# Kernel optimization log

Measured on AMD Instinct MI355X. Metric: run time of the kernel, lower is better.

The kernel has to match this reference:

```python
import jax, jax.numpy as jnp
import numpy as np

HEADS = 16

def setup_inputs() -> dict:
    key = jax.random.key(0)
    k1, k2, k3 = jax.random.split(key, 3)
    b, t, d = 2, 2048, 1024
    x = jax.random.normal(k1, (b, t, d), dtype=jnp.float32)
    w_qkv = jax.random.normal(k2, (d, 3 * d), dtype=jnp.float32) * (d ** -0.5)
    w_out = jax.random.normal(k3, (d, d), dtype=jnp.float32) * (d ** -0.5)
    b_out = jnp.zeros((d,), dtype=jnp.float32)
    return {"x": x, "w_qkv": w_qkv, "w_out": w_out, "b_out": b_out}

def reference(x, w_qkv, w_out, b_out):
    b, t, d = x.shape
    h = HEADS
    dh = d // h
    qkv = x @ w_qkv                      # [b, t, 3d]
    q, k, v = jnp.split(qkv, 3, axis=-1)
    split_heads = lambda a: a.reshape(b, t, h, dh).transpose(0, 2, 1, 3)  # [b,h,t,dh]
    q, k, v = map(split_heads, (q, k, v))
    # NOTE: faithful to source — no 1/sqrt(dh) scaling, causal=False so no mask
    dots = jnp.einsum('bhid,bhjd->bhij', q, k)      # [b,h,t,t]
    attn = jax.nn.softmax(dots, axis=-1)
    out = jnp.einsum('bhjd,bhij->bhid', v, attn)    # [b,h,t,dh]
    out = out.transpose(0, 2, 1, 3).reshape(b, t, d)
    return out @ w_out + b_out
```

## Files before the change

### kernel.cpp

```cpp
#include <hip/hip_runtime.h>
#include <hip/hip_bf16.h>
#include <stdint.h>

typedef __attribute__((ext_vector_type(4))) float f32x4;
typedef __attribute__((ext_vector_type(8))) short bf16x8;

#define MFMA(a, b, c) __builtin_amdgcn_mfma_f32_16x16x32_bf16((a), (b), (c), 0, 0, 0)
#define BAR do { __builtin_amdgcn_s_barrier(); asm volatile("" ::: "memory"); } while (0)

template <int N> __device__ __forceinline__ void waitcnt_vm() {
  if constexpr (N == 0) asm volatile("s_waitcnt vmcnt(0)" ::: "memory");
  else if constexpr (N == 3) asm volatile("s_waitcnt vmcnt(3)" ::: "memory");
  else if constexpr (N == 4) asm volatile("s_waitcnt vmcnt(4)" ::: "memory");
}

__device__ __forceinline__ uint16_t f2b(float f) {
  uint32_t u = __builtin_bit_cast(uint32_t, f);
  uint32_t r = (u + 0x7FFFu + ((u >> 16) & 1u)) >> 16;
  return (uint16_t)r;
}

__device__ __forceinline__ uint32_t cvt_pk_bf16(float lo, float hi) {
  uint32_t r;
  asm("v_cvt_pk_bf16_f32 %0, %1, %2" : "=v"(r) : "v"(lo), "v"(hi));
  return r;
}

__device__ __forceinline__ float fexp2(float x) {
  float r;
  asm("v_exp_f32 %0, %1" : "=v"(r) : "v"(x));
  return r;
}

__device__ __forceinline__ void gld_lds16(const void* g, void* l) {
  __builtin_amdgcn_global_load_lds((const __attribute__((address_space(1))) uint32_t*)g,
                                   (__attribute__((address_space(3))) uint32_t*)l, 16, 0, 0);
}

__device__ __forceinline__ int swz(int r) {
  return (r & 3) | ((((r >> 2) ^ (r >> 3)) & 1) << 2);
}

__global__ __launch_bounds__(256) void cast_bf16(const float* __restrict__ in,
                                                 uint16_t* __restrict__ out, int n) {
  const int i = (blockIdx.x * 256 + threadIdx.x) * 4;
  if (i >= n) return;
  const float4 v = *(const float4*)(in + i);
  ushort4 o;
  o.x = f2b(v.x); o.y = f2b(v.y); o.z = f2b(v.z); o.w = f2b(v.w);
  *(ushort4*)(out + i) = o;
}

__global__ __launch_bounds__(256) void transpose_cast(const float* __restrict__ in,
                                                      uint16_t* __restrict__ out, int R, int C) {
  __shared__ float t_[32][33];
  const int c0 = blockIdx.x * 32, r0 = blockIdx.y * 32;
  const int tx = threadIdx.x & 31, ty = threadIdx.x >> 5;
#pragma unroll
  for (int i = 0; i < 4; i++)
    t_[ty + i * 8][tx] = in[(size_t)(r0 + ty + i * 8) * C + c0 + tx];
  __syncthreads();
#pragma unroll
  for (int i = 0; i < 4; i++)
    out[(size_t)(c0 + ty + i * 8) * R + r0 + tx] = f2b(t_[tx][ty + i * 8]);
}

template <int NOUT, int BN, bool BF16_OUT, bool BIAS, bool SCALEQ, bool VSPLIT>
__global__ __launch_bounds__(256) void gemm_bt(const uint16_t* __restrict__ A,
                                               const uint16_t* __restrict__ Bt,
                                               const float* __restrict__ bias,
                                               void* __restrict__ Cout,
                                               uint16_t* __restrict__ VTout) {
  constexpr int NF = BN / 32;
  constexpr int TILEB = 8192 + BN * 64;
  constexpr int NL = 2 + BN / 64;
  __shared__ __align__(16) char LDS[3 * TILEB];
  const int tid = threadIdx.x;
  const int wave = tid >> 6, lane = tid & 63;
  const int lr = lane & 15, lg = lane >> 4;
  const int row0 = blockIdx.y * 128, col0 = blockIdx.x * BN;
  const int wr = (wave >> 1) * 64, wc = (wave & 1) * (BN / 2);

  f32x4 acc[4][NF] = {};

  const int ldsOff = wave * 1024 + lane * 16;
  const int srow = ldsOff >> 6, scolB = ldsOff & 63;
  const char* ApA = (const char*)A + ((size_t)(row0 + srow) * 1024) * 2 + scolB;
  const char* ApB = ApA + 64 * 2048;
  const char* BpA = (const char*)Bt + ((size_t)(col0 + srow) * 1024) * 2 + scolB;
  const char* BpB = BpA + 64 * 2048;

  auto stage = [&](int t, char* base) {
    char* d = base + wave * 1024;
    const int kk = t * 64;
    gld_lds16(ApA + kk, d);
    gld_lds16(ApB + kk, d + 4096);
    gld_lds16(BpA + kk, d + 8192);
    if constexpr (BN == 128) gld_lds16(BpB + kk, d + 12288);
  };
  auto compute = [&](const char* S) {
    bf16x8 af[4], bfv[NF];
#pragma unroll
    for (int i = 0; i < 4; i++)
      af[i] = *(const bf16x8*)(S + (wr + i * 16 + lr) * 64 + lg * 16);
#pragma unroll
    for (int j = 0; j < NF; j++)
      bfv[j] = *(const bf16x8*)(S + 8192 + (wc + j * 16 + lr) * 64 + lg * 16);
    __builtin_amdgcn_s_setprio(1);
#pragma unroll
    for (int i = 0; i < 4; i++)
#pragma unroll
      for (int j = 0; j < NF; j++)
        acc[i][j] = MFMA(af[i], bfv[j], acc[i][j]);
    __builtin_amdgcn_s_setprio(0);
  };

  stage(0, LDS);
  stage(1, LDS + TILEB);
#pragma unroll 1
  for (int i = 0; i < 30; i += 3) {
    waitcnt_vm<NL>(); BAR; stage(i + 2, LDS + 2 * TILEB); compute(LDS);
    waitcnt_vm<NL>(); BAR; stage(i + 3, LDS);             compute(LDS + TILEB);
    waitcnt_vm<NL>(); BAR; stage(i + 4, LDS + TILEB);     compute(LDS + 2 * TILEB);
  }
  waitcnt_vm<NL>(); BAR; compute(LDS);
  waitcnt_vm<0>();  BAR; compute(LDS + TILEB);

  const float qs = (SCALEQ && col0 < 1024) ? 1.4426950408889634f : 1.0f;
#pragma unroll
  for (int i = 0; i < 4; i++)
#pragma unroll
    for (int j = 0; j < NF; j++) {
      const int col = col0 + wc + j * 16 + lr;
      const int rowb = row0 + wr + i * 16 + lg * 4;
      if (VSPLIT && col >= 2048) {
        ushort4 vs;
        vs.x = f2b(acc[i][j][0]); vs.y = f2b(acc[i][j][1]);
        vs.z = f2b(acc[i][j][2]); vs.w = f2b(acc[i][j][3]);
        const int bIdx = rowb >> 11, tok = rowb & 2047;
        *(ushort4*)(VTout + (size_t)(bIdx * 1024 + (col - 2048)) * 2048 + tok) = vs;
      } else {
        const float bv = BIAS ? bias[col] : 0.f;
#pragma unroll
        for (int r = 0; r < 4; r++) {
          const float v = acc[i][j][r] * qs + bv;
          if (BF16_OUT) ((uint16_t*)Cout)[(size_t)(rowb + r) * NOUT + col] = f2b(v);
          else          ((float*)Cout)[(size_t)(rowb + r) * NOUT + col] = v;
        }
      }
    }
}

__global__ __launch_bounds__(256) void attn_fwd(const uint16_t* __restrict__ qkv,
                                                const uint16_t* __restrict__ VT,
                                                uint16_t* __restrict__ O) {
  __shared__ __align__(16) char LDS[2 * 16384];
  const int tid = threadIdx.x;
  const int wave = tid >> 6, lane = tid & 63;
  const int lr = lane & 15, lg = lane >> 4;
  const int id = blockIdx.x;
  const int w = id >> 3;
  const int bh = (id & 7) * 4 + (w >> 4);
  const int qt = w & 15;
  const int b = bh >> 4, h = bh & 15;
  const int q0 = qt * 128 + wave * 32;

  const uint16_t* Qp = qkv + (size_t)(b * 2048 + q0 + lr) * 3072 + h * 64 + lg * 8;
  const bf16x8 qA0 = *(const bf16x8*)Qp;
  const bf16x8 qA1 = *(const bf16x8*)(Qp + 32);
  const bf16x8 qB0 = *(const bf16x8*)(Qp + 16 * 3072);
  const bf16x8 qB1 = *(const bf16x8*)(Qp + 16 * 3072 + 32);

  const int off1 = wave * 1024 + lane * 16;
  const int off2 = off1 + 4096;
  const int r1 = off1 >> 7, c1 = (off1 >> 4) & 7;
  const int r2 = off2 >> 7, c2 = (off2 >> 4) & 7;
  const char* qb = (const char*)qkv;
  const char* vb = (const char*)VT;
  const char* Kp1 = qb + ((size_t)(b * 2048 + r1) * 3072 + 1024 + h * 64) * 2 + (c1 ^ swz(r1)) * 16;
  const char* Kp2 = qb + ((size_t)(b * 2048 + r2) * 3072 + 1024 + h * 64) * 2 + (c2 ^ swz(r2)) * 16;
  const char* Vp1 = vb + ((size_t)(bh * 64 + r1) * 2048) * 2 + (c1 ^ swz(r1)) * 16;
  const char* Vp2 = vb + ((size_t)(bh * 64 + r2) * 2048) * 2 + (c2 ^ swz(r2)) * 16;

  const int wb1 = wave * 1024;
  const int wb2 = 4096 + wave * 1024;

  auto stage = [&](size_t t, char* slot) {
    const size_t ka = t * 393216;
    const int va = (int)t * 128;
    gld_lds16(Kp1 + ka, slot + wb1);
    gld_lds16(Kp2 + ka, slot + wb2);
    gld_lds16(Vp1 + va, slot + 8192 + wb1);
    gld_lds16(Vp2 + va, slot + 8192 + wb2);
  };

  int koff[8], voff[8];
  const int rbase = ((lr >> 2) << 3) | (lr & 3);
#pragma unroll
  for (int fj = 0; fj < 4; fj++) {
    const int row = rbase + ((fj & 1) << 2) + ((fj >> 1) << 5);
    const int sw = swz(row);
    koff[fj * 2]     = row * 128 + ((lg ^ sw) * 16);
    koff[fj * 2 + 1] = row * 128 + (((4 + lg) ^ sw) * 16);
  }
#pragma unroll
  for (int cf = 0; cf < 4; cf++) {
    const int dr = cf * 16 + lr;
    const int sw = swz(dr);
    voff[cf * 2]     = 8192 + dr * 128 + ((lg ^ sw) * 16);
    voff[cf * 2 + 1] = 8192 + dr * 128 + (((4 + lg) ^ sw) * 16);
  }

  f32x4 oA[4] = {}, oB[4] = {};
  float lA = 0.f, lB = 0.f;
  const char* ldsB = (const char*)LDS;

  union PW { uint32_t u[8]; struct { bf16x8 a0, a1; } f; };

  auto compute = [&](int sb) {
    f32x4 s0[4] = {}, s1[4] = {};
    __builtin_amdgcn_s_setprio(1);
#pragma unroll
    for (int fj = 0; fj < 4; fj++) {
      const bf16x8 k0 = *(const bf16x8*)(ldsB + sb + koff[fj * 2]);
      const bf16x8 k1 = *(const bf16x8*)(ldsB + sb + koff[fj * 2 + 1]);
      s0[fj] = MFMA(k0, qA0, s0[fj]);
      s0[fj] = MFMA(k1, qA1, s0[fj]);
      s1[fj] = MFMA(k0, qB0, s1[fj]);
      s1[fj] = MFMA(k1, qB1, s1[fj]);
    }
    __builtin_amdgcn_s_setprio(0);
    PW pA, pB;
#pragma unroll
    for (int fj = 0; fj < 4; fj++) {
      const float a0 = fexp2(s0[fj][0]), a1 = fexp2(s0[fj][1]);
      const float a2 = fexp2(s0[fj][2]), a3 = fexp2(s0[fj][3]);
      lA += (a0 + a1) + (a2 + a3);
      pA.u[fj * 2]     = cvt_pk_bf16(a0, a1);
      pA.u[fj * 2 + 1] = cvt_pk_bf16(a2, a3);
      const float b0 = fexp2(s1[fj][0]), b1 = fexp2(s1[fj][1]);
      const float b2 = fexp2(s1[fj][2]), b3 = fexp2(s1[fj][3]);
      lB += (b0 + b1) + (b2 + b3);
      pB.u[fj * 2]     = cvt_pk_bf16(b0, b1);
      pB.u[fj * 2 + 1] = cvt_pk_bf16(b2, b3);
    }
    __builtin_amdgcn_s_setprio(1);
#pragma unroll
    for (int cf = 0; cf < 4; cf++) {
      const bf16x8 v0 = *(const bf16x8*)(ldsB + sb + voff[cf * 2]);
      const bf16x8 v1 = *(const bf16x8*)(ldsB + sb + voff[cf * 2 + 1]);
      oA[cf] = MFMA(pA.f.a0, v0, oA[cf]);
      oA[cf] = MFMA(pA.f.a1, v1, oA[cf]);
      oB[cf] = MFMA(pB.f.a0, v0, oB[cf]);
      oB[cf] = MFMA(pB.f.a1, v1, oB[cf]);
    }
    __builtin_amdgcn_s_setprio(0);
  };

  stage(0, LDS);
#pragma unroll 1
  for (int t = 0; t < 30; t += 2) {
    BAR;
    stage(t + 1, LDS + 16384);
    waitcnt_vm<4>(); BAR;
    compute(0);
    BAR;
    stage(t + 2, LDS);
    waitcnt_vm<4>(); BAR;
    compute(16384);
  }
  BAR; stage(31, LDS + 16384);
  waitcnt_vm<4>(); BAR; compute(0);
  waitcnt_vm<0>(); BAR; compute(16384);

  lA += __shfl_xor(lA, 16, 64); lA += __shfl_xor(lA, 32, 64);
  lB += __shfl_xor(lB, 16, 64); lB += __shfl_xor(lB, 32, 64);

#pragma unroll
  for (int cf = 0; cf < 4; cf++)
#pragma unroll
    for (int r = 0; r < 4; r++) {
      const float la = __shfl(lA, lg * 4 + r, 64);
      const float lb = __shfl(lB, lg * 4 + r, 64);
      const int col = h * 64 + cf * 16 + lr;
      const int rowA = b * 2048 + q0 + lg * 4 + r;
      O[(size_t)rowA * 1024 + col] = f2b(oA[cf][r] / la);
      O[(size_t)(rowA + 16) * 1024 + col] = f2b(oB[cf][r] / lb);
    }
}

extern "C" void kernel_launch(void* const* d_in, const int* in_sizes, int n_in,
                              void* d_out, int out_size, void* d_ws, size_t ws_size,
                              hipStream_t stream) {
  const float* x    = (const float*)d_in[0];
  const float* wqkv = (const float*)d_in[1];
  const float* wout = (const float*)d_in[2];
  const float* bout = (const float*)d_in[3];

  char* ws = (char*)d_ws;
  uint16_t* woutT   = (uint16_t*)(ws + 0);
  uint16_t* qkvb    = (uint16_t*)(ws + (2ull  << 20));
  uint16_t* VT      = (uint16_t*)(ws + (26ull << 20));
  uint16_t* xb      = (uint16_t*)(ws + (34ull << 20));
  uint16_t* wqkvT   = (uint16_t*)(ws + (42ull << 20));
  uint16_t* attnout = xb;

  cast_bf16<<<dim3(4096), dim3(256), 0, stream>>>(x, xb, 4096 * 1024);
  transpose_cast<<<dim3(96, 32), dim3(256), 0, stream>>>(wqkv, wqkvT, 1024, 3072);
  transpose_cast<<<dim3(32, 32), dim3(256), 0, stream>>>(wout, woutT, 1024, 1024);

  gemm_bt<3072, 128, true, false, true, true>
      <<<dim3(24, 32), dim3(256), 0, stream>>>(xb, wqkvT, nullptr, qkvb, VT);
  attn_fwd<<<dim3(512), dim3(256), 0, stream>>>(qkvb, VT, attnout);
  gemm_bt<1024, 64, false, true, false, false>
      <<<dim3(16, 32), dim3(256), 0, stream>>>(attnout, woutT, bout, d_out, nullptr);
}
```

Before: 113.8 us.

## Merge prologue kernels and streamline attention softmax row-sum and normalization

Merges the three cast/transpose prologue kernels into one launch that dispatches on block index, removing two kernel launches and their gaps. In the attention kernel, the softmax row-sum now uses packed bf16 dot2 instructions against a vector of ones, replacing scalar float adds. QK accumulators are seeded from a zero constant instead of being zero-initialized each step, and the final division becomes a reciprocal-multiply. Summing the bf16-rounded probabilities changes numerics slightly, though it matches the values actually fed to the PV matmul.

```diff
diff --git a/kernel.cpp b/kernel.cpp
--- a/kernel.cpp
+++ b/kernel.cpp
@@ -32,6 +32,10 @@
   return r;
 }
 
+__device__ __forceinline__ void dot2_acc(float& l, uint32_t p, uint32_t ones2) {
+  asm("v_dot2_f32_bf16 %0, %1, %2, %0" : "+v"(l) : "v"(p), "v"(ones2));
+}
+
 __device__ __forceinline__ void gld_lds16(const void* g, void* l) {
   __builtin_amdgcn_global_load_lds((const __attribute__((address_space(1))) uint32_t*)g,
                                    (__attribute__((address_space(3))) uint32_t*)l, 16, 0, 0);
@@ -41,20 +45,29 @@
   return (r & 3) | ((((r >> 2) ^ (r >> 3)) & 1) << 2);
 }
 
-__global__ __launch_bounds__(256) void cast_bf16(const float* __restrict__ in,
-                                                 uint16_t* __restrict__ out, int n) {
-  const int i = (blockIdx.x * 256 + threadIdx.x) * 4;
-  if (i >= n) return;
-  const float4 v = *(const float4*)(in + i);
-  ushort4 o;
-  o.x = f2b(v.x); o.y = f2b(v.y); o.z = f2b(v.z); o.w = f2b(v.w);
-  *(ushort4*)(out + i) = o;
-}
-
-__global__ __launch_bounds__(256) void transpose_cast(const float* __restrict__ in,
-                                                      uint16_t* __restrict__ out, int R, int C) {
+__global__ __launch_bounds__(256) void prologue(const float* __restrict__ x,
+                                                const float* __restrict__ wqkv,
+                                                const float* __restrict__ wout,
+                                                uint16_t* __restrict__ xb,
+                                                uint16_t* __restrict__ wqkvT,
+                                                uint16_t* __restrict__ woutT) {
   __shared__ float t_[32][33];
-  const int c0 = blockIdx.x * 32, r0 = blockIdx.y * 32;
+  const int bid = blockIdx.x;
+  if (bid < 4096) {
+    const int i = (bid * 256 + threadIdx.x) * 4;
+    const float4 v = *(const float4*)(x + i);
+    ushort4 o;
+    o.x = f2b(v.x); o.y = f2b(v.y); o.z = f2b(v.z); o.w = f2b(v.w);
+    *(ushort4*)(xb + i) = o;
+    return;
+  }
+  const float* in;
+  uint16_t* out;
+  int C, bx, by;
+  if (bid < 7168) { in = wqkv; out = wqkvT; C = 3072; bx = (bid - 4096) % 96; by = (bid - 4096) / 96; }
+  else            { in = wout; out = woutT; C = 1024; bx = (bid - 7168) & 31;  by = (bid - 7168) >> 5; }
+  const int R = 1024;
+  const int c0 = bx * 32, r0 = by * 32;
   const int tx = threadIdx.x & 31, ty = threadIdx.x >> 5;
 #pragma unroll
   for (int i = 0; i < 4; i++)
@@ -212,21 +225,23 @@
   }
 
   f32x4 oA[4] = {}, oB[4] = {};
-  float lA = 0.f, lB = 0.f;
+  float lA0 = 0.f, lA1 = 0.f, lB0 = 0.f, lB1 = 0.f;
+  const uint32_t ones2 = 0x3F803F80u;
+  const f32x4 z4 = {0.f, 0.f, 0.f, 0.f};
   const char* ldsB = (const char*)LDS;
 
   union PW { uint32_t u[8]; struct { bf16x8 a0, a1; } f; };
 
   auto compute = [&](int sb) {
-    f32x4 s0[4] = {}, s1[4] = {};
+    f32x4 s0[4], s1[4];
     __builtin_amdgcn_s_setprio(1);
 #pragma unroll
     for (int fj = 0; fj < 4; fj++) {
       const bf16x8 k0 = *(const bf16x8*)(ldsB + sb + koff[fj * 2]);
       const bf16x8 k1 = *(const bf16x8*)(ldsB + sb + koff[fj * 2 + 1]);
-      s0[fj] = MFMA(k0, qA0, s0[fj]);
+      s0[fj] = MFMA(k0, qA0, z4);
       s0[fj] = MFMA(k1, qA1, s0[fj]);
-      s1[fj] = MFMA(k0, qB0, s1[fj]);
+      s1[fj] = MFMA(k0, qB0, z4);
       s1[fj] = MFMA(k1, qB1, s1[fj]);
     }
     __builtin_amdgcn_s_setprio(0);
@@ -235,14 +250,19 @@
     for (int fj = 0; fj < 4; fj++) {
       const float a0 = fexp2(s0[fj][0]), a1 = fexp2(s0[fj][1]);
       const float a2 = fexp2(s0[fj][2]), a3 = fexp2(s0[fj][3]);
-      lA += (a0 + a1) + (a2 + a3);
       pA.u[fj * 2]     = cvt_pk_bf16(a0, a1);
       pA.u[fj * 2 + 1] = cvt_pk_bf16(a2, a3);
       const float b0 = fexp2(s1[fj][0]), b1 = fexp2(s1[fj][1]);
       const float b2 = fexp2(s1[fj][2]), b3 = fexp2(s1[fj][3]);
-      lB += (b0 + b1) + (b2 + b3);
       pB.u[fj * 2]     = cvt_pk_bf16(b0, b1);
       pB.u[fj * 2 + 1] = cvt_pk_bf16(b2, b3);
+    }
+#pragma unroll
+    for (int j = 0; j < 8; j += 2) {
+      dot2_acc(lA0, pA.u[j], ones2);
+      dot2_acc(lA1, pA.u[j + 1], ones2);
+      dot2_acc(lB0, pB.u[j], ones2);
+      dot2_acc(lB1, pB.u[j + 1], ones2);
     }
     __builtin_amdgcn_s_setprio(1);
 #pragma unroll
@@ -273,19 +293,24 @@
   waitcnt_vm<4>(); BAR; compute(0);
   waitcnt_vm<0>(); BAR; compute(16384);
 
+  float lA = lA0 + lA1, lB = lB0 + lB1;
   lA += __shfl_xor(lA, 16, 64); lA += __shfl_xor(lA, 32, 64);
   lB += __shfl_xor(lB, 16, 64); lB += __shfl_xor(lB, 32, 64);
 
+  float invA[4], invB[4];
+#pragma unroll
+  for (int r = 0; r < 4; r++) {
+    invA[r] = 1.0f / __shfl(lA, lg * 4 + r, 64);
+    invB[r] = 1.0f / __shfl(lB, lg * 4 + r, 64);
+  }
 #pragma unroll
   for (int cf = 0; cf < 4; cf++)
 #pragma unroll
     for (int r = 0; r < 4; r++) {
-      const float la = __shfl(lA, lg * 4 + r, 64);
-      const float lb = __shfl(lB, lg * 4 + r, 64);
       const int col = h * 64 + cf * 16 + lr;
       const int rowA = b * 2048 + q0 + lg * 4 + r;
-      O[(size_t)rowA * 1024 + col] = f2b(oA[cf][r] / la);
-      O[(size_t)(rowA + 16) * 1024 + col] = f2b(oB[cf][r] / lb);
+      O[(size_t)rowA * 1024 + col] = f2b(oA[cf][r] * invA[r]);
+      O[(size_t)(rowA + 16) * 1024 + col] = f2b(oB[cf][r] * invB[r]);
     }
 }
 
@@ -305,9 +330,7 @@
   uint16_t* wqkvT   = (uint16_t*)(ws + (42ull << 20));
   uint16_t* attnout = xb;
 
-  cast_bf16<<<dim3(4096), dim3(256), 0, stream>>>(x, xb, 4096 * 1024);
-  transpose_cast<<<dim3(96, 32), dim3(256), 0, stream>>>(wqkv, wqkvT, 1024, 3072);
-  transpose_cast<<<dim3(32, 32), dim3(256), 0, stream>>>(wout, woutT, 1024, 1024);
+  prologue<<<dim3(8192), dim3(256), 0, stream>>>(x, wqkv, wout, xb, wqkvT, woutT);
 
   gemm_bt<3072, 128, true, false, true, true>
       <<<dim3(24, 32), dim3(256), 0, stream>>>(xb, wqkvT, nullptr, qkvb, VT);
```

Result: faster. 108.0 us (-5.1%).
